# Kernel optimization log

Measured on AMD Instinct MI355X. Metric: run time of the kernel, lower is better.

Reference implementation:

```python
import jax, jax.numpy as jnp
import numpy as np

N_NODES = 100000
N_EDGES = 1000000
IN_FEAT = 128
OUT_FEAT = 128
NUM_RELS = 64
NUM_BASES = 16
SUBMAT_IN = IN_FEAT // NUM_BASES   # 8
SUBMAT_OUT = OUT_FEAT // NUM_BASES # 8


def setup_inputs() -> dict:
    key = jax.random.key(0)
    k = jax.random.split(key, 8)
    h = jax.random.normal(k[0], (N_NODES, IN_FEAT), dtype=jnp.float32)
    norm = jax.random.uniform(k[1], (N_EDGES, 1), dtype=jnp.float32)
    src = jax.random.randint(k[2], (N_EDGES,), 0, N_NODES, dtype=jnp.int32)
    dst = jax.random.randint(k[3], (N_EDGES,), 0, N_NODES, dtype=jnp.int32)
    r = jax.random.randint(k[4], (N_EDGES,), 0, NUM_RELS, dtype=jnp.int32)
    # learned params (xavier-uniform style scale)
    wscale = np.sqrt(6.0 / (SUBMAT_IN + SUBMAT_OUT)) * np.sqrt(2.0)
    weight = jax.random.uniform(k[5], (NUM_RELS, NUM_BASES * SUBMAT_IN * SUBMAT_OUT),
                                minval=-wscale, maxval=wscale, dtype=jnp.float32)
    lscale = np.sqrt(6.0 / (IN_FEAT + OUT_FEAT)) * np.sqrt(2.0)
    loop_weight = jax.random.uniform(k[6], (IN_FEAT, OUT_FEAT),
                                     minval=-lscale, maxval=lscale, dtype=jnp.float32)
    h_bias = jnp.zeros((OUT_FEAT,), dtype=jnp.float32)
    return {"h": h, "norm": norm, "weight": weight, "loop_weight": loop_weight,
            "h_bias": h_bias, "src": src, "dst": dst, "r": r}


def reference(h, norm, weight, loop_weight, h_bias, src, dst, r):
    E = src.shape[0]
    # per-edge block-diagonal weights: (E, B, si, so)
    w = weight[r].reshape(E, NUM_BASES, SUBMAT_IN, SUBMAT_OUT)
    # src features split into blocks: (E, B, si)
    hs = h[src].reshape(E, NUM_BASES, SUBMAT_IN)
    # small bmm per block, flatten to (E, OUT_FEAT)
    msg = jnp.einsum('ebi,ebio->ebo', hs, w).reshape(E, OUT_FEAT)
    msg = msg * norm
    # scatter-sum to destination nodes
    agg = jax.ops.segment_sum(msg, dst, num_segments=N_NODES)
    # self-loop message (dropout=0.0) + bias
    out = agg + h_bias + h @ loop_weight
    return jax.nn.relu(out)
```

## Files before the change

### kernel.cpp

```cpp
#include <hip/hip_runtime.h>
#include <stdint.h>

#define N_NODES 100000
#define N_EDGES 1000000
#define IN_F 128
#define OUT_F 128
#define NUM_RELS 64
#define NB_SCAN ((N_NODES + 255) / 256)
#define N_WAVES 16384

typedef _Float16 half2v __attribute__((ext_vector_type(2)));

__device__ __forceinline__ float dot2f(uint32_t hu, uint32_t wu, float acc) {
#if __has_builtin(__builtin_amdgcn_fdot2)
    return __builtin_amdgcn_fdot2(__builtin_bit_cast(half2v, hu),
                                  __builtin_bit_cast(half2v, wu), acc, false);
#else
    half2v a = __builtin_bit_cast(half2v, hu);
    half2v b = __builtin_bit_cast(half2v, wu);
    acc = fmaf((float)a.x, (float)b.x, acc);
    acc = fmaf((float)a.y, (float)b.y, acc);
    return acc;
#endif
}

__device__ __forceinline__ uint32_t pkh2(float x, float y) {
    half2v v;
    v.x = (_Float16)x;
    v.y = (_Float16)y;
    return __builtin_bit_cast(uint32_t, v);
}

__global__ __launch_bounds__(256) void gemm_selfloop(
    const float* __restrict__ h, const float* __restrict__ W,
    const float* __restrict__ bias, float* __restrict__ out, int n_nodes)
{
    const int tid = threadIdx.x;
    const int ty = tid >> 4, tx = tid & 15;
    const int node0 = blockIdx.x * 128 + ty * 8;
    const int o0 = tx * 8;

    float acc[8][8];
#pragma unroll
    for (int j = 0; j < 8; ++j)
#pragma unroll
        for (int i = 0; i < 8; ++i) acc[j][i] = 0.f;

    int nidx[8];
#pragma unroll
    for (int j = 0; j < 8; ++j) {
        int n = node0 + j;
        nidx[j] = n < n_nodes ? n : (n_nodes - 1);
    }

    for (int k = 0; k < IN_F; k += 4) {
        float hsv[8][4];
#pragma unroll
        for (int j = 0; j < 8; ++j) {
            float4 hv = *reinterpret_cast<const float4*>(h + (size_t)nidx[j] * IN_F + k);
            *reinterpret_cast<float4*>(hsv[j]) = hv;
        }
#pragma unroll
        for (int kk = 0; kk < 4; ++kk) {
            const float* wrow = W + (size_t)(k + kk) * OUT_F + o0;
            float wr[8];
            *reinterpret_cast<float4*>(wr)     = *reinterpret_cast<const float4*>(wrow);
            *reinterpret_cast<float4*>(wr + 4) = *reinterpret_cast<const float4*>(wrow + 4);
#pragma unroll
            for (int j = 0; j < 8; ++j) {
                const float hk = hsv[j][kk];
#pragma unroll
                for (int i = 0; i < 8; ++i)
                    acc[j][i] = fmaf(hk, wr[i], acc[j][i]);
            }
        }
    }

    float br[8];
    *reinterpret_cast<float4*>(br)     = *reinterpret_cast<const float4*>(bias + o0);
    *reinterpret_cast<float4*>(br + 4) = *reinterpret_cast<const float4*>(bias + o0 + 4);

#pragma unroll
    for (int j = 0; j < 8; ++j) {
        int n = node0 + j;
        if (n < n_nodes) {
            float4 v0, v1;
            v0.x = acc[j][0] + br[0]; v0.y = acc[j][1] + br[1];
            v0.z = acc[j][2] + br[2]; v0.w = acc[j][3] + br[3];
            v1.x = acc[j][4] + br[4]; v1.y = acc[j][5] + br[5];
            v1.z = acc[j][6] + br[6]; v1.w = acc[j][7] + br[7];
            float* op = out + (size_t)n * OUT_F + o0;
            *reinterpret_cast<float4*>(op)     = v0;
            *reinterpret_cast<float4*>(op + 4) = v1;
        }
    }
}

__global__ __launch_bounds__(256) void prep_hist_h16(
    const float* __restrict__ weight, uint32_t* __restrict__ wsw,
    const int* __restrict__ dst, int* __restrict__ cnt,
    const float* __restrict__ h, uint4* __restrict__ h16_4,
    int n_edges, int do_h16)
{
    int t = blockIdx.x * 256 + threadIdx.x;
    if (t < NUM_RELS * 512) {
        int r  = t >> 9;
        int w9 = t & 511;
        int k  = w9 >> 6;
        int l  = w9 & 63;
        int b  = l >> 2;
        int q  = l & 3;
        int ip = k >> 1;
        int oc = k & 1;
        int o  = 2 * q + oc;
        const float* s = weight + (size_t)r * 1024 + b * 64 + (2 * ip) * 8 + o;
        half2v v;
        v.x = (_Float16)s[0];
        v.y = (_Float16)s[8];
        wsw[t] = __builtin_bit_cast(uint32_t, v);
        return;
    }
    int e = t - NUM_RELS * 512;
    if (e < n_edges) {
        atomicAdd(&cnt[dst[e]], 1);
        return;
    }
    if (!do_h16) return;
    int t2 = e - n_edges;
    if (t2 < N_NODES * IN_F / 8) {
        const float4* hp = reinterpret_cast<const float4*>(h + (size_t)t2 * 8);
        float4 a = hp[0], c = hp[1];
        uint4 r;
        r.x = pkh2(a.x, a.y);
        r.y = pkh2(a.z, a.w);
        r.z = pkh2(c.x, c.y);
        r.w = pkh2(c.z, c.w);
        h16_4[t2] = r;
    }
}

__global__ __launch_bounds__(256) void block_sums(
    const int* __restrict__ cnt, int* __restrict__ part, int n)
{
    __shared__ int sdata[256];
    int i = blockIdx.x * 256 + threadIdx.x;
    sdata[threadIdx.x] = (i < n) ? cnt[i] : 0;
    __syncthreads();
    for (int s = 128; s > 0; s >>= 1) {
        if (threadIdx.x < s) sdata[threadIdx.x] += sdata[threadIdx.x + s];
        __syncthreads();
    }
    if (threadIdx.x == 0) part[blockIdx.x] = sdata[0];
}

__global__ __launch_bounds__(512) void scan_partials(int* __restrict__ part, int nb)
{
    __shared__ int buf[512];
    int tid = threadIdx.x;
    int v = (tid < nb) ? part[tid] : 0;
    buf[tid] = v;
    __syncthreads();
    for (int ofs = 1; ofs < 512; ofs <<= 1) {
        int t = (tid >= ofs) ? buf[tid - ofs] : 0;
        __syncthreads();
        buf[tid] += t;
        __syncthreads();
    }
    if (tid < nb) part[tid] = buf[tid] - v;
}

__global__ __launch_bounds__(256) void write_off(
    const int* __restrict__ cnt, const int* __restrict__ part,
    int* __restrict__ off, int* __restrict__ cur, int n, int n_edges)
{
    __shared__ int buf[256];
    int tid = threadIdx.x;
    int i = blockIdx.x * 256 + tid;
    int v = (i < n) ? cnt[i] : 0;
    buf[tid] = v;
    __syncthreads();
    for (int ofs = 1; ofs < 256; ofs <<= 1) {
        int t = (tid >= ofs) ? buf[tid - ofs] : 0;
        __syncthreads();
        buf[tid] += t;
        __syncthreads();
    }
    int excl = buf[tid] - v + part[blockIdx.x];
    if (i < n) { off[i] = excl; cur[i] = excl; }
    if (i == n - 1) off[n] = n_edges;
}

__global__ __launch_bounds__(256) void fill_and_part(
    const int* __restrict__ src, const int* __restrict__ dst,
    const int* __restrict__ rel, const float* __restrict__ norm,
    int* __restrict__ cur, int2* __restrict__ emeta,
    const int* __restrict__ off, int* __restrict__ wstart, int n_edges)
{
    int t = blockIdx.x * 256 + threadIdx.x;
    if (t < n_edges) {
        int d = dst[t];
        int p = atomicAdd(&cur[d], 1);
        int2 m;
        m.x = src[t] | (rel[t] << 20);
        m.y = __float_as_int(norm[t]);
        emeta[p] = m;
    } else {
        int w = t - n_edges;
        if (w <= N_WAVES) {
            if (w == 0) {
                wstart[0] = 0;
            } else if (w == N_WAVES) {
                wstart[N_WAVES] = N_NODES;
            } else {
                int target = (int)(((long long)N_EDGES * w) / N_WAVES);
                int lo = 0, hi = N_NODES - 1;
                while (lo < hi) {
                    int mid = (lo + hi) >> 1;
                    if (off[mid + 1] > target) hi = mid; else lo = mid + 1;
                }
                wstart[w] = lo;
            }
        }
    }
}

__global__ __launch_bounds__(1024, 4) void gather_nodes7(
    const uint4* __restrict__ h16_4, const uint32_t* __restrict__ wsw,
    const int* __restrict__ off, const int2* __restrict__ emeta,
    const int* __restrict__ wstart, float* __restrict__ out)
{
    __shared__ uint32_t wlds[NUM_RELS * 512];

    {
        uint4* l4 = reinterpret_cast<uint4*>(wlds);
        const uint4* g4 = reinterpret_cast<const uint4*>(wsw);
        int t = threadIdx.x;
#pragma unroll
        for (int k = 0; k < 8; ++k)
            l4[t + k * 1024] = g4[t + k * 1024];
    }
    __syncthreads();

    const int lane = threadIdx.x & 63;
    const int wid  = threadIdx.x >> 6;
    const int wv   = blockIdx.x * 16 + wid;
    const int b = lane >> 2;
    const int q = lane & 3;

    const int n0 = wstart[wv];
    const int n1 = wstart[wv + 1];
    if (n0 >= n1) return;

    int j = off[n0];
    int e_next = off[n0 + 1];

    int2 m0 = emeta[j];
    int2 m1 = emeta[j + 1];
    int2 m2 = emeta[j + 2];
    uint4 hv0 = h16_4[((uint32_t)m0.x & 0xFFFFFu) * 16 + b];
    uint4 hv1 = h16_4[((uint32_t)m1.x & 0xFFFFFu) * 16 + b];

    uint32_t base = ((uint32_t)m0.x >> 20) * 512 + (uint32_t)lane;
    uint32_t w0 = wlds[base],       w1 = wlds[base + 64];
    uint32_t w2 = wlds[base + 128], w3 = wlds[base + 192];
    uint32_t w4 = wlds[base + 256], w5 = wlds[base + 320];
    uint32_t w6 = wlds[base + 384], w7 = wlds[base + 448];

    for (int d = n0; d < n1; ++d) {
        const int idx2 = (d + 2 < n1) ? d + 2 : n1;
        const int e_nn = off[idx2];
        float a0 = 0.f, a1 = 0.f;

        while (j < e_next) {
            int2 m3 = emeta[j + 3];
            uint4 hv2 = h16_4[((uint32_t)m2.x & 0xFFFFFu) * 16 + b];
            uint32_t bn = ((uint32_t)m1.x >> 20) * 512 + (uint32_t)lane;
            uint32_t wn0 = wlds[bn],       wn1 = wlds[bn + 64];
            uint32_t wn2 = wlds[bn + 128], wn3 = wlds[bn + 192];
            uint32_t wn4 = wlds[bn + 256], wn5 = wlds[bn + 320];
            uint32_t wn6 = wlds[bn + 384], wn7 = wlds[bn + 448];

            float s0 = dot2f(hv0.x, w0, 0.f);
            s0 = dot2f(hv0.y, w2, s0);
            s0 = dot2f(hv0.z, w4, s0);
            s0 = dot2f(hv0.w, w6, s0);
            float s1 = dot2f(hv0.x, w1, 0.f);
            s1 = dot2f(hv0.y, w3, s1);
            s1 = dot2f(hv0.z, w5, s1);
            s1 = dot2f(hv0.w, w7, s1);

            const float nm = __int_as_float(m0.y);
            a0 = fmaf(s0, nm, a0);
            a1 = fmaf(s1, nm, a1);

            m0 = m1; m1 = m2; m2 = m3;
            hv0 = hv1; hv1 = hv2;
            w0 = wn0; w1 = wn1; w2 = wn2; w3 = wn3;
            w4 = wn4; w5 = wn5; w6 = wn6; w7 = wn7;
            ++j;
        }

        float2* op = reinterpret_cast<float2*>(out + (size_t)d * OUT_F + b * 8 + 2 * q);
        float2 bse = *op;
        float2 res;
        res.x = fmaxf(bse.x + a0, 0.f);
        res.y = fmaxf(bse.y + a1, 0.f);
        *op = res;

        e_next = e_nn;
    }
}

__global__ __launch_bounds__(1024, 4) void gather_nodes6(
    const float* __restrict__ h, const uint32_t* __restrict__ wsw,
    const int* __restrict__ off, const int2* __restrict__ emeta,
    const int* __restrict__ wstart, float* __restrict__ out)
{
    __shared__ uint32_t wlds[NUM_RELS * 512];
    {
        uint4* l4 = reinterpret_cast<uint4*>(wlds);
        const uint4* g4 = reinterpret_cast<const uint4*>(wsw);
        int t = threadIdx.x;
#pragma unroll
        for (int k = 0; k < 8; ++k)
            l4[t + k * 1024] = g4[t + k * 1024];
    }
    __syncthreads();

    const int lane = threadIdx.x & 63;
    const int wid  = threadIdx.x >> 6;
    const int wv   = blockIdx.x * 16 + wid;
    const int b = lane >> 2;
    const int q = lane & 3;

    const int n0 = wstart[wv];
    const int n1 = wstart[wv + 1];
    if (n0 >= n1) return;

    int j = off[n0];
    int2 m0 = emeta[j];
    int2 m1 = emeta[j + 1];
    int2 m2 = emeta[j + 2];

    const float4* hr0 = reinterpret_cast<const float4*>(
        h + (size_t)((uint32_t)m0.x & 0xFFFFFu) * IN_F + b * 8);
    float4 h0A = hr0[0], h0B = hr0[1];
    const float4* hr1 = reinterpret_cast<const float4*>(
        h + (size_t)((uint32_t)m1.x & 0xFFFFFu) * IN_F + b * 8);
    float4 h1A = hr1[0], h1B = hr1[1];

    uint32_t base = ((uint32_t)m0.x >> 20) * 512 + (uint32_t)lane;
    uint32_t w0 = wlds[base],       w1 = wlds[base + 64];
    uint32_t w2 = wlds[base + 128], w3 = wlds[base + 192];
    uint32_t w4 = wlds[base + 256], w5 = wlds[base + 320];
    uint32_t w6 = wlds[base + 384], w7 = wlds[base + 448];

    for (int d = n0; d < n1; ++d) {
        const int end_d = off[d + 1];
        float a0 = 0.f, a1 = 0.f;

        while (j < end_d) {
            int2 m3 = emeta[j + 3];
            const float4* hr2 = reinterpret_cast<const float4*>(
                h + (size_t)((uint32_t)m2.x & 0xFFFFFu) * IN_F + b * 8);
            float4 h2A = hr2[0], h2B = hr2[1];
            uint32_t bn = ((uint32_t)m1.x >> 20) * 512 + (uint32_t)lane;
            uint32_t wn0 = wlds[bn],       wn1 = wlds[bn + 64];
            uint32_t wn2 = wlds[bn + 128], wn3 = wlds[bn + 192];
            uint32_t wn4 = wlds[bn + 256], wn5 = wlds[bn + 320];
            uint32_t wn6 = wlds[bn + 384], wn7 = wlds[bn + 448];

            uint32_t h01 = __builtin_bit_cast(uint32_t, __builtin_amdgcn_cvt_pkrtz(h0A.x, h0A.y));
            uint32_t h23 = __builtin_bit_cast(uint32_t, __builtin_amdgcn_cvt_pkrtz(h0A.z, h0A.w));
            uint32_t h45 = __builtin_bit_cast(uint32_t, __builtin_amdgcn_cvt_pkrtz(h0B.x, h0B.y));
            uint32_t h67 = __builtin_bit_cast(uint32_t, __builtin_amdgcn_cvt_pkrtz(h0B.z, h0B.w));

            float s0 = dot2f(h01, w0, 0.f);
            s0 = dot2f(h23, w2, s0);
            s0 = dot2f(h45, w4, s0);
            s0 = dot2f(h67, w6, s0);
            float s1 = dot2f(h01, w1, 0.f);
            s1 = dot2f(h23, w3, s1);
            s1 = dot2f(h45, w5, s1);
            s1 = dot2f(h67, w7, s1);

            const float nm = __int_as_float(m0.y);
            a0 = fmaf(s0, nm, a0);
            a1 = fmaf(s1, nm, a1);

            m0 = m1; m1 = m2; m2 = m3;
            h0A = h1A; h0B = h1B; h1A = h2A; h1B = h2B;
            w0 = wn0; w1 = wn1; w2 = wn2; w3 = wn3;
            w4 = wn4; w5 = wn5; w6 = wn6; w7 = wn7;
            ++j;
        }

        float2* op = reinterpret_cast<float2*>(out + (size_t)d * OUT_F + b * 8 + 2 * q);
        float2 bse = *op;
        float2 res;
        res.x = fmaxf(bse.x + a0, 0.f);
        res.y = fmaxf(bse.y + a1, 0.f);
        *op = res;
    }
}

extern "C" void kernel_launch(void* const* d_in, const int* in_sizes, int n_in,
                              void* d_out, int out_size, void* d_ws, size_t ws_size,
                              hipStream_t stream)
{
    const float* h      = (const float*)d_in[0];
    const float* norm   = (const float*)d_in[1];
    const float* weight = (const float*)d_in[2];
    const float* loop_w = (const float*)d_in[3];
    const float* bias   = (const float*)d_in[4];
    const int*   src    = (const int*)d_in[5];
    const int*   dst    = (const int*)d_in[6];
    const int*   rel    = (const int*)d_in[7];
    float* out = (float*)d_out;

    char* wsb = (char*)d_ws;
    char* ws0 = wsb;
    int*  cnt    = (int*)wsb;  wsb += sizeof(int) * N_NODES;
    int*  off    = (int*)wsb;  wsb += sizeof(int) * (N_NODES + 1);
    int*  cur    = (int*)wsb;  wsb += sizeof(int) * N_NODES;
    int*  part   = (int*)wsb;  wsb += sizeof(int) * 512;
    int*  wstart = (int*)wsb;  wsb += sizeof(int) * (N_WAVES + 1);
    wsb = (char*)(((uintptr_t)wsb + 15) & ~(uintptr_t)15);
    uint32_t* wsw = (uint32_t*)wsb; wsb += sizeof(uint32_t) * NUM_RELS * 512;
    int2* emeta = (int2*)wsb;  wsb += sizeof(int2) * (N_EDGES + 3);
    wsb = (char*)(((uintptr_t)wsb + 15) & ~(uintptr_t)15);
    uint4* h16_4 = (uint4*)wsb; wsb += (size_t)N_NODES * IN_F * 2;

    const int use_h16 = (size_t)(wsb - ws0) <= ws_size;

    hipMemsetAsync(cnt, 0, sizeof(int) * N_NODES, stream);
    hipMemsetAsync(emeta + N_EDGES, 0, 3 * sizeof(int2), stream);

    const int h16_threads = use_h16 ? (N_NODES * IN_F / 8) : 0;
    const int ph_grid = (NUM_RELS * 512 + N_EDGES + h16_threads + 255) / 256;
    prep_hist_h16<<<ph_grid, 256, 0, stream>>>(weight, wsw, dst, cnt,
                                               h, h16_4, N_EDGES, use_h16);
    block_sums<<<NB_SCAN, 256, 0, stream>>>(cnt, part, N_NODES);
    scan_partials<<<1, 512, 0, stream>>>(part, NB_SCAN);
    write_off<<<NB_SCAN, 256, 0, stream>>>(cnt, part, off, cur, N_NODES, N_EDGES);
    const int fp_grid = (N_EDGES + N_WAVES + 1 + 255) / 256;
    fill_and_part<<<fp_grid, 256, 0, stream>>>(src, dst, rel, norm, cur, emeta,
                                               off, wstart, N_EDGES);

    gemm_selfloop<<<(N_NODES + 127) / 128, 256, 0, stream>>>(h, loop_w, bias, out, N_NODES);
    if (use_h16) {
        gather_nodes7<<<1024, 1024, 0, stream>>>(h16_4, wsw, off, emeta, wstart, out);
    } else {
        gather_nodes6<<<1024, 1024, 0, stream>>>(h, wsw, off, emeta, wstart, out);
    }
}
```

Baseline: 333.5 us.

## Flatten per-node gather loop into 4-deep edge pipeline and fuse partial scan

The gather kernel now walks the wave's edge range as one flat stream, unrolled by four. It keeps four edges of metadata, half-precision features and LDS weights in flight, and flushes node outputs inline when an edge index crosses a node boundary. This is meant to deepen memory-level parallelism and to remove the per-node loop overhead and pipeline restart. The separate single-block partial-sum scan kernel is removed; each write_off block now reduces the preceding block sums itself, which drops one launch at the cost of redundant reads. Edge metadata padding grows to 8 entries to cover the deeper prefetch.

New measurement: 352.8 us. +5.8%, slower.

```diff
diff --git a/kernel.cpp b/kernel.cpp
--- a/kernel.cpp
+++ b/kernel.cpp
@@ -153,29 +153,26 @@
     if (threadIdx.x == 0) part[blockIdx.x] = sdata[0];
 }
 
-__global__ __launch_bounds__(512) void scan_partials(int* __restrict__ part, int nb)
-{
-    __shared__ int buf[512];
-    int tid = threadIdx.x;
-    int v = (tid < nb) ? part[tid] : 0;
-    buf[tid] = v;
-    __syncthreads();
-    for (int ofs = 1; ofs < 512; ofs <<= 1) {
-        int t = (tid >= ofs) ? buf[tid - ofs] : 0;
-        __syncthreads();
-        buf[tid] += t;
-        __syncthreads();
-    }
-    if (tid < nb) part[tid] = buf[tid] - v;
-}
-
-__global__ __launch_bounds__(256) void write_off(
+__global__ __launch_bounds__(256) void write_off2(
     const int* __restrict__ cnt, const int* __restrict__ part,
     int* __restrict__ off, int* __restrict__ cur, int n, int n_edges)
 {
+    __shared__ int sdata[256];
     __shared__ int buf[256];
-    int tid = threadIdx.x;
-    int i = blockIdx.x * 256 + tid;
+    const int tid = threadIdx.x;
+    const int bid = blockIdx.x;
+
+    int psum = 0;
+    for (int t = tid; t < bid; t += 256) psum += part[t];
+    sdata[tid] = psum;
+    __syncthreads();
+    for (int s = 128; s > 0; s >>= 1) {
+        if (tid < s) sdata[tid] += sdata[tid + s];
+        __syncthreads();
+    }
+    const int blockoff = sdata[0];
+
+    int i = bid * 256 + tid;
     int v = (i < n) ? cnt[i] : 0;
     buf[tid] = v;
     __syncthreads();
@@ -185,7 +182,7 @@
         buf[tid] += t;
         __syncthreads();
     }
-    int excl = buf[tid] - v + part[blockIdx.x];
+    int excl = buf[tid] - v + blockoff;
     if (i < n) { off[i] = excl; cur[i] = excl; }
     if (i == n - 1) off[n] = n_edges;
 }
@@ -224,7 +221,7 @@
     }
 }
 
-__global__ __launch_bounds__(1024, 4) void gather_nodes7(
+__global__ __launch_bounds__(1024, 4) void gather_nodes8(
     const uint4* __restrict__ h16_4, const uint32_t* __restrict__ wsw,
     const int* __restrict__ off, const int2* __restrict__ emeta,
     const int* __restrict__ wstart, float* __restrict__ out)
@@ -251,64 +248,79 @@
     const int n1 = wstart[wv + 1];
     if (n0 >= n1) return;
 
-    int j = off[n0];
-    int e_next = off[n0 + 1];
-
-    int2 m0 = emeta[j];
-    int2 m1 = emeta[j + 1];
-    int2 m2 = emeta[j + 2];
-    uint4 hv0 = h16_4[((uint32_t)m0.x & 0xFFFFFu) * 16 + b];
-    uint4 hv1 = h16_4[((uint32_t)m1.x & 0xFFFFFu) * 16 + b];
-
-    uint32_t base = ((uint32_t)m0.x >> 20) * 512 + (uint32_t)lane;
-    uint32_t w0 = wlds[base],       w1 = wlds[base + 64];
-    uint32_t w2 = wlds[base + 128], w3 = wlds[base + 192];
-    uint32_t w4 = wlds[base + 256], w5 = wlds[base + 320];
-    uint32_t w6 = wlds[base + 384], w7 = wlds[base + 448];
-
-    for (int d = n0; d < n1; ++d) {
-        const int idx2 = (d + 2 < n1) ? d + 2 : n1;
-        const int e_nn = off[idx2];
-        float a0 = 0.f, a1 = 0.f;
-
-        while (j < e_next) {
-            int2 m3 = emeta[j + 3];
-            uint4 hv2 = h16_4[((uint32_t)m2.x & 0xFFFFFu) * 16 + b];
-            uint32_t bn = ((uint32_t)m1.x >> 20) * 512 + (uint32_t)lane;
-            uint32_t wn0 = wlds[bn],       wn1 = wlds[bn + 64];
-            uint32_t wn2 = wlds[bn + 128], wn3 = wlds[bn + 192];
-            uint32_t wn4 = wlds[bn + 256], wn5 = wlds[bn + 320];
-            uint32_t wn6 = wlds[bn + 384], wn7 = wlds[bn + 448];
-
-            float s0 = dot2f(hv0.x, w0, 0.f);
-            s0 = dot2f(hv0.y, w2, s0);
-            s0 = dot2f(hv0.z, w4, s0);
-            s0 = dot2f(hv0.w, w6, s0);
-            float s1 = dot2f(hv0.x, w1, 0.f);
-            s1 = dot2f(hv0.y, w3, s1);
-            s1 = dot2f(hv0.z, w5, s1);
-            s1 = dot2f(hv0.w, w7, s1);
-
-            const float nm = __int_as_float(m0.y);
+    int d  = n0;
+    int j  = off[n0];
+    const int je = off[n1];
+    int en1 = off[d + 1];
+    int en2 = off[(d + 2 <= n1) ? d + 2 : n1];
+
+    float a0 = 0.f, a1 = 0.f;
+
+    auto flush_node = [&]() {
+        float2* op = reinterpret_cast<float2*>(out + (size_t)d * OUT_F + b * 8 + 2 * q);
+        float2 bs = *op;
+        float2 r;
+        r.x = fmaxf(bs.x + a0, 0.f);
+        r.y = fmaxf(bs.y + a1, 0.f);
+        *op = r;
+        a0 = 0.f; a1 = 0.f;
+        ++d;
+        en1 = en2;
+        en2 = off[(d + 2 <= n1) ? d + 2 : n1];
+    };
+
+    auto step = [&](int2& m, uint4& hv, uint32_t (&w)[8], int jj) {
+        while (jj == en1 && d < n1) flush_node();
+        if (jj < je) {
+            float s0 = dot2f(hv.x, w[0], 0.f);
+            s0 = dot2f(hv.y, w[2], s0);
+            s0 = dot2f(hv.z, w[4], s0);
+            s0 = dot2f(hv.w, w[6], s0);
+            float s1 = dot2f(hv.x, w[1], 0.f);
+            s1 = dot2f(hv.y, w[3], s1);
+            s1 = dot2f(hv.z, w[5], s1);
+            s1 = dot2f(hv.w, w[7], s1);
+            const float nm = __int_as_float(m.y);
             a0 = fmaf(s0, nm, a0);
             a1 = fmaf(s1, nm, a1);
-
-            m0 = m1; m1 = m2; m2 = m3;
-            hv0 = hv1; hv1 = hv2;
-            w0 = wn0; w1 = wn1; w2 = wn2; w3 = wn3;
-            w4 = wn4; w5 = wn5; w6 = wn6; w7 = wn7;
-            ++j;
-        }
-
-        float2* op = reinterpret_cast<float2*>(out + (size_t)d * OUT_F + b * 8 + 2 * q);
-        float2 bse = *op;
-        float2 res;
-        res.x = fmaxf(bse.x + a0, 0.f);
-        res.y = fmaxf(bse.y + a1, 0.f);
-        *op = res;
-
-        e_next = e_nn;
-    }
+        }
+        int2 mn = emeta[jj + 4];
+        m = mn;
+        hv = h16_4[((uint32_t)mn.x & 0xFFFFFu) * 16 + b];
+        uint32_t bs = ((uint32_t)mn.x >> 20) * 512 + (uint32_t)lane;
+#pragma unroll
+        for (int i = 0; i < 8; ++i) w[i] = wlds[bs + i * 64];
+    };
+
+    int2 mA = emeta[j],     mB = emeta[j + 1];
+    int2 mC = emeta[j + 2], mD = emeta[j + 3];
+    uint4 hA = h16_4[((uint32_t)mA.x & 0xFFFFFu) * 16 + b];
+    uint4 hB = h16_4[((uint32_t)mB.x & 0xFFFFFu) * 16 + b];
+    uint4 hC = h16_4[((uint32_t)mC.x & 0xFFFFFu) * 16 + b];
+    uint4 hD = h16_4[((uint32_t)mD.x & 0xFFFFFu) * 16 + b];
+    uint32_t wA[8], wB[8], wC[8], wD[8];
+    {
+        uint32_t bsA = ((uint32_t)mA.x >> 20) * 512 + (uint32_t)lane;
+        uint32_t bsB = ((uint32_t)mB.x >> 20) * 512 + (uint32_t)lane;
+        uint32_t bsC = ((uint32_t)mC.x >> 20) * 512 + (uint32_t)lane;
+        uint32_t bsD = ((uint32_t)mD.x >> 20) * 512 + (uint32_t)lane;
+#pragma unroll
+        for (int i = 0; i < 8; ++i) {
+            wA[i] = wlds[bsA + i * 64];
+            wB[i] = wlds[bsB + i * 64];
+            wC[i] = wlds[bsC + i * 64];
+            wD[i] = wlds[bsD + i * 64];
+        }
+    }
+
+    for (; j < je; j += 4) {
+        step(mA, hA, wA, j);
+        step(mB, hB, wB, j + 1);
+        step(mC, hC, wC, j + 2);
+        step(mD, hD, wD, j + 3);
+    }
+
+    while (d < n1) flush_node();
 }
 
 __global__ __launch_bounds__(1024, 4) void gather_nodes6(
@@ -427,29 +439,28 @@
     int*  wstart = (int*)wsb;  wsb += sizeof(int) * (N_WAVES + 1);
     wsb = (char*)(((uintptr_t)wsb + 15) & ~(uintptr_t)15);
     uint32_t* wsw = (uint32_t*)wsb; wsb += sizeof(uint32_t) * NUM_RELS * 512;
-    int2* emeta = (int2*)wsb;  wsb += sizeof(int2) * (N_EDGES + 3);
+    int2* emeta = (int2*)wsb;  wsb += sizeof(int2) * (N_EDGES + 8);
     wsb = (char*)(((uintptr_t)wsb + 15) & ~(uintptr_t)15);
     uint4* h16_4 = (uint4*)wsb; wsb += (size_t)N_NODES * IN_F * 2;
 
     const int use_h16 = (size_t)(wsb - ws0) <= ws_size;
 
     hipMemsetAsync(cnt, 0, sizeof(int) * N_NODES, stream);
-    hipMemsetAsync(emeta + N_EDGES, 0, 3 * sizeof(int2), stream);
+    hipMemsetAsync(emeta + N_EDGES, 0, 8 * sizeof(int2), stream);
 
     const int h16_threads = use_h16 ? (N_NODES * IN_F / 8) : 0;
     const int ph_grid = (NUM_RELS * 512 + N_EDGES + h16_threads + 255) / 256;
     prep_hist_h16<<<ph_grid, 256, 0, stream>>>(weight, wsw, dst, cnt,
                                                h, h16_4, N_EDGES, use_h16);
     block_sums<<<NB_SCAN, 256, 0, stream>>>(cnt, part, N_NODES);
-    scan_partials<<<1, 512, 0, stream>>>(part, NB_SCAN);
-    write_off<<<NB_SCAN, 256, 0, stream>>>(cnt, part, off, cur, N_NODES, N_EDGES);
+    write_off2<<<NB_SCAN, 256, 0, stream>>>(cnt, part, off, cur, N_NODES, N_EDGES);
     const int fp_grid = (N_EDGES + N_WAVES + 1 + 255) / 256;
     fill_and_part<<<fp_grid, 256, 0, stream>>>(src, dst, rel, norm, cur, emeta,
                                                off, wstart, N_EDGES);
 
     gemm_selfloop<<<(N_NODES + 127) / 128, 256, 0, stream>>>(h, loop_w, bias, out, N_NODES);
     if (use_h16) {
-        gather_nodes7<<<1024, 1024, 0, stream>>>(h16_4, wsw, off, emeta, wstart, out);
+        gather_nodes8<<<1024, 1024, 0, stream>>>(h16_4, wsw, off, emeta, wstart, out);
     } else {
         gather_nodes6<<<1024, 1024, 0, stream>>>(h, wsw, off, emeta, wstart, out);
     }
```
